# Optimization experiments

Hardware: AMD Instinct MI355X
Metric: run time of the kernel (lower is better)

Reference implementation:

```python
import jax, jax.numpy as jnp
import numpy as np

B, SQ, SKV, D, H = 2, 2048, 2048, 1024, 16
DH = D // H


def setup_inputs() -> dict:
    key = jax.random.key(0)
    ks = jax.random.split(key, 4)
    s = 0.02
    return {
        "query_input": jax.random.normal(ks[0], (B, SQ, D), jnp.float32),
        "kv_input": jax.random.normal(ks[1], (B, SKV, D), jnp.float32),
        "Wq": jax.random.normal(ks[2], (D, D), jnp.float32) * s,
        "bq": jnp.zeros((D,), jnp.float32),
        "Wkv": jax.random.normal(ks[3], (D, 2 * D), jnp.float32) * s,
        "bkv": jnp.zeros((2 * D,), jnp.float32),
        "Wo": jax.random.normal(jax.random.fold_in(key, 7), (D, D), jnp.float32) * s,
        "bo": jnp.zeros((D,), jnp.float32),
    }


def reference(query_input, kv_input, Wq, bq, Wkv, bkv, Wo, bo):
    scale = 1.0 / jnp.sqrt(jnp.float32(DH))
    # Projections
    q = query_input @ Wq + bq                      # [B, SQ, D]
    kv = kv_input @ Wkv + bkv                      # [B, SKV, 2D]
    k, v = jnp.split(kv, 2, axis=-1)               # [B, SKV, D] each
    # Split heads: [B, H, S, DH]
    q = q.reshape(B, SQ, H, DH).transpose(0, 2, 1, 3)
    k = k.reshape(B, SKV, H, DH).transpose(0, 2, 1, 3)
    v = v.reshape(B, SKV, H, DH).transpose(0, 2, 1, 3)
    # Scores S = QK^T / sqrt(d_k)
    scores = jnp.einsum("bhqd,bhkd->bhqk", q, k) * scale
    attn = jax.nn.softmax(scores, axis=-1)
    out = jnp.einsum("bhqk,bhkd->bhqd", attn, v)   # [B, H, SQ, DH]
    out = out.transpose(0, 2, 1, 3).reshape(B, SQ, D)
    return out @ Wo + bo
```

## Files before the change

### kernel.cpp

```cpp
#include <hip/hip_runtime.h>

typedef unsigned short u16;
typedef unsigned int u32;
typedef __bf16 bf16x8 __attribute__((ext_vector_type(8)));
typedef __bf16 bf16x2 __attribute__((ext_vector_type(2)));
typedef float f32x4 __attribute__((ext_vector_type(4)));

#define QSCALE 0.18033688011112f

__device__ __forceinline__ u16 f2bf(float f) {
  u32 u = __builtin_bit_cast(u32, f);
  u += 0x7fffu + ((u >> 16) & 1u);
  return (u16)(u >> 16);
}

__device__ __forceinline__ u32 pkbf(float a, float b) {
  bf16x2 t = {(__bf16)a, (__bf16)b};
  return __builtin_bit_cast(u32, t);
}

__device__ __forceinline__ bf16x8 as_bf16x8(uint4 v) {
  return __builtin_bit_cast(bf16x8, v);
}

__device__ __forceinline__ void async16(const void* g, void* l) {
  __builtin_amdgcn_global_load_lds(
      (__attribute__((address_space(1))) void*)(g),
      (__attribute__((address_space(3))) void*)(l), 16, 0, 0);
}

__global__ void prep_kernel(const float* __restrict__ xq, const float* __restrict__ xkv,
                            const float* __restrict__ Wq, const float* __restrict__ Wkv,
                            const float* __restrict__ Wo,
                            u16* __restrict__ Xq16, u16* __restrict__ Xkv16,
                            u16* __restrict__ WqT, u16* __restrict__ WkvT,
                            u16* __restrict__ WoT) {
  const int bid = blockIdx.x, tid = threadIdx.x;
  if (bid < 8192) {
    int i = bid * 256 + tid;
    const float* s; u16* d; int j;
    if (i < 1048576) { s = xq; d = Xq16; j = i; }
    else             { s = xkv; d = Xkv16; j = i - 1048576; }
    float4 v = ((const float4*)s)[j];
    ushort4 o;
    o.x = f2bf(v.x); o.y = f2bf(v.y); o.z = f2bf(v.z); o.w = f2bf(v.w);
    ((ushort4*)d)[j] = o;
    return;
  }
  const int b2 = bid - 8192;
  const int z = b2 >> 11, rem = b2 & 2047;
  const int by = rem >> 6, bx = rem & 63;
  const float* src; u16* dst; int Nd;
  if (z == 0)      { src = Wq;  dst = WqT;  Nd = 1024; }
  else if (z == 1) { src = Wkv; dst = WkvT; Nd = 2048; }
  else             { src = Wo;  dst = WoT;  Nd = 1024; }
  const int n0 = bx * 32, k0 = by * 32;
  if (n0 >= Nd) return;
  __shared__ float tile[32][33];
  const int tx = tid & 31, ty = tid >> 5;
#pragma unroll
  for (int j = 0; j < 4; ++j)
    tile[ty + 8 * j][tx] = src[(size_t)(k0 + ty + 8 * j) * Nd + n0 + tx];
  __syncthreads();
#pragma unroll
  for (int j = 0; j < 4; ++j)
    dst[(size_t)(n0 + ty + 8 * j) * 1024 + k0 + tx] = f2bf(tile[tx][ty + 8 * j]);
}

template <int MI>
static __device__ __forceinline__ void gemm_core(
    const u16* __restrict__ A, const u16* __restrict__ Bt, int m0,
    uint4* sA, uint4* sB, f32x4 (*acc)[4]) {
  const int tid = threadIdx.x;
  const int wv = tid >> 6, lane = tid & 63;
  const int quad = lane >> 4, l16 = lane & 15;
  const int wm = (wv >> 1) * (MI * 16), wn = (wv & 1) * 64;

  const int ib0 = wv * 128 + lane, ib1 = ib0 + 64;
  const int br0 = ib0 >> 2, bc0 = (ib0 & 3) ^ ((br0 >> 1) & 3);
  const int br1 = ib1 >> 2, bc1 = (ib1 & 3) ^ ((br1 >> 1) & 3);
  const u16* gB0 = Bt + (size_t)br0 * 1024 + bc0 * 8;
  const u16* gB1 = Bt + (size_t)br1 * 1024 + bc1 * 8;

  const int ia0 = wv * (MI * 32) + lane;
  const int ar0 = ia0 >> 2, ac0 = (ia0 & 3) ^ ((ar0 >> 1) & 3);
  const u16* gA0 = A + (size_t)(m0 + ar0) * 1024 + ac0 * 8;
  const int ia1 = ia0 + 64;
  const int ar1 = ia1 >> 2, ac1 = (ia1 & 3) ^ ((ar1 >> 1) & 3);
  const u16* gA1 = A + (size_t)(m0 + ar1) * 1024 + ac1 * 8;
  uint4* sAw = sA + wv * (MI * 32);
  uint4* sBw = sB + wv * 128;

  for (int k0 = 0; k0 < 1024; k0 += 32) {
    __syncthreads();
    async16(gA0 + k0, sAw);
    if (MI == 4) async16(gA1 + k0, sAw + 64);
    async16(gB0 + k0, sBw);
    async16(gB1 + k0, sBw + 64);
    __syncthreads();

    bf16x8 af[MI], bfr[4];
#pragma unroll
    for (int mi = 0; mi < MI; ++mi) {
      int r = wm + mi * 16 + l16;
      af[mi] = as_bf16x8(sA[r * 4 + (quad ^ ((r >> 1) & 3))]);
    }
#pragma unroll
    for (int ni = 0; ni < 4; ++ni) {
      int r = wn + ni * 16 + l16;
      bfr[ni] = as_bf16x8(sB[r * 4 + (quad ^ ((r >> 1) & 3))]);
    }
#pragma unroll
    for (int mi = 0; mi < MI; ++mi)
#pragma unroll
      for (int ni = 0; ni < 4; ++ni)
        acc[mi][ni] = __builtin_amdgcn_mfma_f32_16x16x32_bf16(
            af[mi], bfr[ni], acc[mi][ni], 0, 0, 0);
  }
}

__global__ __launch_bounds__(256, 3) void gemm_qkv(
    const u16* __restrict__ Xq, const u16* __restrict__ Xkv,
    const u16* __restrict__ WqT, const u16* __restrict__ WkvT,
    const float* __restrict__ bq, const float* __restrict__ bkv,
    u16* __restrict__ Qd, u16* __restrict__ Kd, u16* __restrict__ Vd) {
  __shared__ uint4 sA[512], sB[512];
  f32x4 acc[4][4] = {};
  const int n0 = blockIdx.x * 128, m0 = blockIdx.y * 128;
  const u16* A = (n0 < 1024) ? Xq : Xkv;
  const u16* Bt = (n0 < 1024) ? (WqT + (size_t)n0 * 1024)
                              : (WkvT + (size_t)(n0 - 1024) * 1024);
  const float* bias = (n0 < 1024) ? (bq + n0) : (bkv + (n0 - 1024));
  gemm_core<4>(A, Bt, m0, sA, sB, acc);

  const int tid = threadIdx.x, wv = tid >> 6, lane = tid & 63;
  const int quad = lane >> 4, l16 = lane & 15;
  const int wm = (wv >> 1) * 64, wn = (wv & 1) * 64;
  const int bb = m0 >> 11;
  const int gmb = m0 + wm + quad * 4;
  const int ssb = (m0 & 2047) + wm + quad * 4;
#pragma unroll
  for (int ni = 0; ni < 4; ++ni) {
    const int gn = n0 + wn + ni * 16 + l16;
    const float bvn = bias[wn + ni * 16 + l16];
    if (gn < 1024) {
      u16* base = Qd + gn;
#pragma unroll
      for (int mi = 0; mi < 4; ++mi)
#pragma unroll
        for (int r = 0; r < 4; ++r)
          base[(size_t)(gmb + mi * 16 + r) * 1024] = f2bf((acc[mi][ni][r] + bvn) * QSCALE);
    } else if (gn < 2048) {
      u16* base = Kd + (gn - 1024);
#pragma unroll
      for (int mi = 0; mi < 4; ++mi)
#pragma unroll
        for (int r = 0; r < 4; ++r)
          base[(size_t)(gmb + mi * 16 + r) * 1024] = f2bf(acc[mi][ni][r] + bvn);
    } else {
      const int col = gn - 2048, hh = col >> 6, dh = col & 63;
      u16* base = Vd + ((size_t)(bb * 16 + hh) * 64 + dh) * 2048 + ssb;
#pragma unroll
      for (int mi = 0; mi < 4; ++mi) {
        ushort4 o;
        o.x = f2bf(acc[mi][ni][0] + bvn);
        o.y = f2bf(acc[mi][ni][1] + bvn);
        o.z = f2bf(acc[mi][ni][2] + bvn);
        o.w = f2bf(acc[mi][ni][3] + bvn);
        *(ushort4*)(base + mi * 16) = o;
      }
    }
  }
}

__global__ __launch_bounds__(256, 2) void flash_attn(
    const u16* __restrict__ Q, const u16* __restrict__ K,
    const u16* __restrict__ V, u16* __restrict__ O) {
  __shared__ uint4 sK[2][512];
  __shared__ uint4 sV[2][512];
  __shared__ __align__(16) u16 sP[4][32][72];

  const int tid = threadIdx.x;
  const int wv = tid >> 6, lane = tid & 63;
  const int quad = lane >> 4, l16 = lane & 15;
  const int hb = blockIdx.x & 31;
  const int q0 = (blockIdx.x >> 5) * 128;
  const int h = hb & 15, bz = hb >> 4;

  const u16* Qb = Q + ((size_t)(bz * 2048 + q0)) * 1024 + h * 64;
  const u16* Kb = K + ((size_t)(bz * 2048)) * 1024 + h * 64;
  const u16* Vb = V + ((size_t)(bz * 16 + h)) * 64 * 2048;

  bf16x8 qf[2][2];
#pragma unroll
  for (int rb = 0; rb < 2; ++rb) {
    const uint4* qp = (const uint4*)(Qb + (size_t)(wv * 32 + rb * 16 + l16) * 1024);
    qf[rb][0] = as_bf16x8(qp[quad]);
    qf[rb][1] = as_bf16x8(qp[4 + quad]);
  }

  f32x4 oacc[2][4] = {};
  f32x4 lsum[2] = {};
  const uint4 ones4 = {0x3F803F80u, 0x3F803F80u, 0x3F803F80u, 0x3F803F80u};
  const bf16x8 ones = as_bf16x8(ones4);

  const int i0 = wv * 128 + lane, i1 = i0 + 64;
  const int kr0 = i0 >> 3, kr1 = i1 >> 3;
  const int kck0 = (i0 & 7) ^ ((i0 >> 5) & 7);
  const int kck1 = (i1 & 7) ^ ((i1 >> 5) & 7);
  const int vck0 = (i0 & 7) ^ (kr0 & 7);
  const int vck1 = (i1 & 7) ^ (kr1 & 7);
  const u16* gK0 = Kb + (size_t)kr0 * 1024 + kck0 * 8;
  const u16* gK1 = Kb + (size_t)kr1 * 1024 + kck1 * 8;
  const u16* gV0 = Vb + (size_t)kr0 * 2048 + vck0 * 8;
  const u16* gV1 = Vb + (size_t)kr1 * 2048 + vck1 * 8;
  const int wo = wv * 128;

  async16(gK0, &sK[0][wo]);
  async16(gK1, &sK[0][wo + 64]);
  async16(gV0, &sV[0][wo]);
  async16(gV1, &sV[0][wo + 64]);

  for (int t = 0; t < 32; ++t) {
    const int cur = t & 1;
    __syncthreads();
    if (t < 31) {
      const int nxt = cur ^ 1;
      const size_t ko = (size_t)(t + 1) * 64 * 1024;
      const int vo = (t + 1) * 64;
      async16(gK0 + ko, &sK[nxt][wo]);
      async16(gK1 + ko, &sK[nxt][wo + 64]);
      async16(gV0 + vo, &sV[nxt][wo]);
      async16(gV1 + vo, &sV[nxt][wo + 64]);
    }
    const uint4* K_ = sK[cur];
    const uint4* V_ = sV[cur];

    bf16x8 bK0[4], bK1[4], vf0[4], vf1[4];
#pragma unroll
    for (int ni = 0; ni < 4; ++ni) {
      int rr = l16 * 4 + ni;
      bK0[ni] = as_bf16x8(K_[rr * 8 + (quad ^ (l16 & 7))]);
      bK1[ni] = as_bf16x8(K_[rr * 8 + ((4 + quad) ^ (l16 & 7))]);
      int vv = ni * 16 + l16;
      vf0[ni] = as_bf16x8(V_[vv * 8 + (quad ^ (vv & 7))]);
      vf1[ni] = as_bf16x8(V_[vv * 8 + ((4 + quad) ^ (vv & 7))]);
    }

#pragma unroll
    for (int rb = 0; rb < 2; ++rb) {
      f32x4 s4[4];
#pragma unroll
      for (int ni = 0; ni < 4; ++ni) {
        f32x4 a = {0.f, 0.f, 0.f, 0.f};
        a = __builtin_amdgcn_mfma_f32_16x16x32_bf16(qf[rb][0], bK0[ni], a, 0, 0, 0);
        a = __builtin_amdgcn_mfma_f32_16x16x32_bf16(qf[rb][1], bK1[ni], a, 0, 0, 0);
        s4[ni] = a;
      }
#pragma unroll
      for (int r = 0; r < 4; ++r) {
        uint2 pk;
        pk.x = pkbf(exp2f(s4[0][r]), exp2f(s4[1][r]));
        pk.y = pkbf(exp2f(s4[2][r]), exp2f(s4[3][r]));
        *(uint2*)&sP[wv][rb * 16 + quad * 4 + r][l16 * 4] = pk;
      }
    }
#pragma unroll
    for (int rb = 0; rb < 2; ++rb) {
      bf16x8 pf0 = as_bf16x8(*(const uint4*)&sP[wv][rb * 16 + l16][quad * 8]);
      bf16x8 pf1 = as_bf16x8(*(const uint4*)&sP[wv][rb * 16 + l16][32 + quad * 8]);
      lsum[rb] = __builtin_amdgcn_mfma_f32_16x16x32_bf16(pf0, ones, lsum[rb], 0, 0, 0);
      lsum[rb] = __builtin_amdgcn_mfma_f32_16x16x32_bf16(pf1, ones, lsum[rb], 0, 0, 0);
#pragma unroll
      for (int ni = 0; ni < 4; ++ni) {
        oacc[rb][ni] = __builtin_amdgcn_mfma_f32_16x16x32_bf16(pf0, vf0[ni], oacc[rb][ni], 0, 0, 0);
        oacc[rb][ni] = __builtin_amdgcn_mfma_f32_16x16x32_bf16(pf1, vf1[ni], oacc[rb][ni], 0, 0, 0);
      }
    }
  }

#pragma unroll
  for (int rb = 0; rb < 2; ++rb) {
    u16* Ob = O + ((size_t)(bz * 2048 + q0 + wv * 32 + rb * 16 + quad * 4)) * 1024
                + h * 64;
#pragma unroll
    for (int r = 0; r < 4; ++r) {
      float rl = 1.0f / lsum[rb][r];
#pragma unroll
      for (int ni = 0; ni < 4; ++ni)
        Ob[(size_t)r * 1024 + ni * 16 + l16] = f2bf(oacc[rb][ni][r] * rl);
    }
  }
}

__global__ __launch_bounds__(256, 2) void gemm_out(
    const u16* __restrict__ A, const u16* __restrict__ Bt,
    const float* __restrict__ bias, float* __restrict__ C) {
  __shared__ uint4 sA[256], sB[512];
  f32x4 acc[2][4] = {};
  const int n0 = blockIdx.x * 128, m0 = blockIdx.y * 64;
  gemm_core<2>(A, Bt + (size_t)n0 * 1024, m0, sA, sB, acc);

  const int tid = threadIdx.x, wv = tid >> 6, lane = tid & 63;
  const int quad = lane >> 4, l16 = lane & 15;
  const int wm = (wv >> 1) * 32, wn = (wv & 1) * 64;
  float bv[4];
#pragma unroll
  for (int ni = 0; ni < 4; ++ni) bv[ni] = bias[n0 + wn + ni * 16 + l16];
#pragma unroll
  for (int mi = 0; mi < 2; ++mi)
#pragma unroll
    for (int ni = 0; ni < 4; ++ni)
#pragma unroll
      for (int r = 0; r < 4; ++r) {
        int gm = m0 + wm + mi * 16 + quad * 4 + r;
        int gn = n0 + wn + ni * 16 + l16;
        C[(size_t)gm * 1024 + gn] = acc[mi][ni][r] + bv[ni];
      }
}

extern "C" void kernel_launch(void* const* d_in, const int* in_sizes, int n_in,
                              void* d_out, int out_size, void* d_ws, size_t ws_size,
                              hipStream_t stream) {
  const float* xq  = (const float*)d_in[0];
  const float* xkv = (const float*)d_in[1];
  const float* Wq  = (const float*)d_in[2];
  const float* bq  = (const float*)d_in[3];
  const float* Wkv = (const float*)d_in[4];
  const float* bkv = (const float*)d_in[5];
  const float* Wo  = (const float*)d_in[6];
  const float* bo  = (const float*)d_in[7];
  float* out = (float*)d_out;

  char* p = (char*)d_ws;
  u16* Xq16  = (u16*)p; p += (size_t)8 << 20;
  u16* Xkv16 = (u16*)p; p += (size_t)8 << 20;
  u16* WqT   = (u16*)p; p += (size_t)2 << 20;
  u16* WkvT  = (u16*)p; p += (size_t)4 << 20;
  u16* WoT   = (u16*)p; p += (size_t)2 << 20;
  u16* Q16   = (u16*)p; p += (size_t)8 << 20;
  u16* K16   = (u16*)p; p += (size_t)8 << 20;
  u16* Vt16  = (u16*)p; p += (size_t)8 << 20;
  u16* O16   = (u16*)p; p += (size_t)8 << 20;

  prep_kernel<<<14336, 256, 0, stream>>>(xq, xkv, Wq, Wkv, Wo,
                                         Xq16, Xkv16, WqT, WkvT, WoT);
  gemm_qkv<<<dim3(24, 32), 256, 0, stream>>>(Xq16, Xkv16, WqT, WkvT, bq, bkv,
                                             Q16, K16, Vt16);
  flash_attn<<<512, 256, 0, stream>>>(Q16, K16, Vt16, O16);
  gemm_out<<<dim3(8, 64), 256, 0, stream>>>(O16, WoT, bo, out);
}
```

Measured before the change: 210.2 us.

## Software-pipeline PV matmul one tile behind QK and exp in flash attention

Restructures the attention loop so the P·V MFMAs for the previous KV tile run while the current tile's QK scores are exponentiated. P is double-buffered in shared memory and the V fragments are carried in registers across iterations. s_setprio is raised around the MFMA block, and the loop is unrolled by two. The aim is to overlap the transcendental and VALU work with matrix-core work, at the cost of more registers (extra V fragments) and more LDS, which may reduce occupancy.

```diff
diff --git a/kernel.cpp b/kernel.cpp
--- a/kernel.cpp
+++ b/kernel.cpp
@@ -178,7 +178,7 @@
     const u16* __restrict__ V, u16* __restrict__ O) {
   __shared__ uint4 sK[2][512];
   __shared__ uint4 sV[2][512];
-  __shared__ __align__(16) u16 sP[4][32][72];
+  __shared__ __align__(16) u16 sP[2][4][32][72];
 
   const int tid = threadIdx.x;
   const int wv = tid >> 6, lane = tid & 63;
@@ -221,6 +221,9 @@
   async16(gV0, &sV[0][wo]);
   async16(gV1, &sV[0][wo + 64]);
 
+  bf16x8 vfp0[4], vfp1[4];
+
+#pragma unroll 2
   for (int t = 0; t < 32; ++t) {
     const int cur = t & 1;
     __syncthreads();
@@ -236,48 +239,76 @@
     const uint4* K_ = sK[cur];
     const uint4* V_ = sV[cur];
 
-    bf16x8 bK0[4], bK1[4], vf0[4], vf1[4];
-#pragma unroll
-    for (int ni = 0; ni < 4; ++ni) {
-      int rr = l16 * 4 + ni;
-      bK0[ni] = as_bf16x8(K_[rr * 8 + (quad ^ (l16 & 7))]);
-      bK1[ni] = as_bf16x8(K_[rr * 8 + ((4 + quad) ^ (l16 & 7))]);
-      int vv = ni * 16 + l16;
-      vf0[ni] = as_bf16x8(V_[vv * 8 + (quad ^ (vv & 7))]);
-      vf1[ni] = as_bf16x8(V_[vv * 8 + ((4 + quad) ^ (vv & 7))]);
-    }
-
-#pragma unroll
-    for (int rb = 0; rb < 2; ++rb) {
-      f32x4 s4[4];
+    bf16x8 vn0[4], vn1[4];
+    f32x4 s4[2][4];
+    {
+      bf16x8 bK0[4], bK1[4];
 #pragma unroll
       for (int ni = 0; ni < 4; ++ni) {
-        f32x4 a = {0.f, 0.f, 0.f, 0.f};
-        a = __builtin_amdgcn_mfma_f32_16x16x32_bf16(qf[rb][0], bK0[ni], a, 0, 0, 0);
-        a = __builtin_amdgcn_mfma_f32_16x16x32_bf16(qf[rb][1], bK1[ni], a, 0, 0, 0);
-        s4[ni] = a;
-      }
+        int rr = l16 * 4 + ni;
+        bK0[ni] = as_bf16x8(K_[rr * 8 + (quad ^ (l16 & 7))]);
+        bK1[ni] = as_bf16x8(K_[rr * 8 + ((4 + quad) ^ (l16 & 7))]);
+        int vv = ni * 16 + l16;
+        vn0[ni] = as_bf16x8(V_[vv * 8 + (quad ^ (vv & 7))]);
+        vn1[ni] = as_bf16x8(V_[vv * 8 + ((4 + quad) ^ (vv & 7))]);
+      }
+
+#pragma unroll
+      for (int rb = 0; rb < 2; ++rb)
+#pragma unroll
+        for (int ni = 0; ni < 4; ++ni) {
+          f32x4 a = {0.f, 0.f, 0.f, 0.f};
+          a = __builtin_amdgcn_mfma_f32_16x16x32_bf16(qf[rb][0], bK0[ni], a, 0, 0, 0);
+          a = __builtin_amdgcn_mfma_f32_16x16x32_bf16(qf[rb][1], bK1[ni], a, 0, 0, 0);
+          s4[rb][ni] = a;
+        }
+    }
+
+    if (t) {
+      __builtin_amdgcn_s_setprio(1);
+#pragma unroll
+      for (int rb = 0; rb < 2; ++rb) {
+        bf16x8 pf0 = as_bf16x8(*(const uint4*)&sP[cur ^ 1][wv][rb * 16 + l16][quad * 8]);
+        bf16x8 pf1 = as_bf16x8(*(const uint4*)&sP[cur ^ 1][wv][rb * 16 + l16][32 + quad * 8]);
+        lsum[rb] = __builtin_amdgcn_mfma_f32_16x16x32_bf16(pf0, ones, lsum[rb], 0, 0, 0);
+        lsum[rb] = __builtin_amdgcn_mfma_f32_16x16x32_bf16(pf1, ones, lsum[rb], 0, 0, 0);
+#pragma unroll
+        for (int ni = 0; ni < 4; ++ni) {
+          oacc[rb][ni] = __builtin_amdgcn_mfma_f32_16x16x32_bf16(pf0, vfp0[ni], oacc[rb][ni], 0, 0, 0);
+          oacc[rb][ni] = __builtin_amdgcn_mfma_f32_16x16x32_bf16(pf1, vfp1[ni], oacc[rb][ni], 0, 0, 0);
+        }
+      }
+      __builtin_amdgcn_s_setprio(0);
+    }
+
+#pragma unroll
+    for (int rb = 0; rb < 2; ++rb)
 #pragma unroll
       for (int r = 0; r < 4; ++r) {
         uint2 pk;
-        pk.x = pkbf(exp2f(s4[0][r]), exp2f(s4[1][r]));
-        pk.y = pkbf(exp2f(s4[2][r]), exp2f(s4[3][r]));
-        *(uint2*)&sP[wv][rb * 16 + quad * 4 + r][l16 * 4] = pk;
-      }
-    }
-#pragma unroll
-    for (int rb = 0; rb < 2; ++rb) {
-      bf16x8 pf0 = as_bf16x8(*(const uint4*)&sP[wv][rb * 16 + l16][quad * 8]);
-      bf16x8 pf1 = as_bf16x8(*(const uint4*)&sP[wv][rb * 16 + l16][32 + quad * 8]);
-      lsum[rb] = __builtin_amdgcn_mfma_f32_16x16x32_bf16(pf0, ones, lsum[rb], 0, 0, 0);
-      lsum[rb] = __builtin_amdgcn_mfma_f32_16x16x32_bf16(pf1, ones, lsum[rb], 0, 0, 0);
-#pragma unroll
-      for (int ni = 0; ni < 4; ++ni) {
-        oacc[rb][ni] = __builtin_amdgcn_mfma_f32_16x16x32_bf16(pf0, vf0[ni], oacc[rb][ni], 0, 0, 0);
-        oacc[rb][ni] = __builtin_amdgcn_mfma_f32_16x16x32_bf16(pf1, vf1[ni], oacc[rb][ni], 0, 0, 0);
-      }
-    }
-  }
+        pk.x = pkbf(exp2f(s4[rb][0][r]), exp2f(s4[rb][1][r]));
+        pk.y = pkbf(exp2f(s4[rb][2][r]), exp2f(s4[rb][3][r]));
+        *(uint2*)&sP[cur][wv][rb * 16 + quad * 4 + r][l16 * 4] = pk;
+      }
+
+#pragma unroll
+    for (int ni = 0; ni < 4; ++ni) { vfp0[ni] = vn0[ni]; vfp1[ni] = vn1[ni]; }
+  }
+
+  __builtin_amdgcn_s_setprio(1);
+#pragma unroll
+  for (int rb = 0; rb < 2; ++rb) {
+    bf16x8 pf0 = as_bf16x8(*(const uint4*)&sP[1][wv][rb * 16 + l16][quad * 8]);
+    bf16x8 pf1 = as_bf16x8(*(const uint4*)&sP[1][wv][rb * 16 + l16][32 + quad * 8]);
+    lsum[rb] = __builtin_amdgcn_mfma_f32_16x16x32_bf16(pf0, ones, lsum[rb], 0, 0, 0);
+    lsum[rb] = __builtin_amdgcn_mfma_f32_16x16x32_bf16(pf1, ones, lsum[rb], 0, 0, 0);
+#pragma unroll
+    for (int ni = 0; ni < 4; ++ni) {
+      oacc[rb][ni] = __builtin_amdgcn_mfma_f32_16x16x32_bf16(pf0, vfp0[ni], oacc[rb][ni], 0, 0, 0);
+      oacc[rb][ni] = __builtin_amdgcn_mfma_f32_16x16x32_bf16(pf1, vfp1[ni], oacc[rb][ni], 0, 0, 0);
+    }
+  }
+  __builtin_amdgcn_s_setprio(0);
 
 #pragma unroll
   for (int rb = 0; rb < 2; ++rb) {
```

After: 207.1 us. About the same (-1.5%).

## Warp-specialize flash attention into QK/softmax producers and PV consumer waves

Applied to the files above, without the earlier changes.

Doubles the flash attention block to 512 threads. Four waves load K and compute QK^T plus exp into a double-buffered P tile, while four other waves load V and run the PV and row-sum MFMAs one tile behind at raised priority. The aim is to overlap the exp/softmax work with the PV matrix multiplies across waves. In exchange it adds shared memory for the second P buffer, needs an extra drain step after the loop, and with 512 blocks of 512 threads on the device it may lower the number of resident blocks.

```diff
diff --git a/kernel.cpp b/kernel.cpp
--- a/kernel.cpp
+++ b/kernel.cpp
@@ -173,15 +173,17 @@
   }
 }
 
-__global__ __launch_bounds__(256, 2) void flash_attn(
+__global__ __launch_bounds__(512, 4) void flash_attn(
     const u16* __restrict__ Q, const u16* __restrict__ K,
     const u16* __restrict__ V, u16* __restrict__ O) {
   __shared__ uint4 sK[2][512];
   __shared__ uint4 sV[2][512];
-  __shared__ __align__(16) u16 sP[4][32][72];
+  __shared__ __align__(16) u16 sP[2][4][32][72];
 
   const int tid = threadIdx.x;
   const int wv = tid >> 6, lane = tid & 63;
+  const int wg = wv & 3;
+  const bool prod = wv < 4;
   const int quad = lane >> 4, l16 = lane & 15;
   const int hb = blockIdx.x & 31;
   const int q0 = (blockIdx.x >> 5) * 128;
@@ -191,84 +193,121 @@
   const u16* Kb = K + ((size_t)(bz * 2048)) * 1024 + h * 64;
   const u16* Vb = V + ((size_t)(bz * 16 + h)) * 64 * 2048;
 
+  const int i0 = wg * 128 + lane, i1 = i0 + 64;
+  const int kr0 = i0 >> 3, kr1 = i1 >> 3;
+  const int wo = wg * 128;
+
   bf16x8 qf[2][2];
-#pragma unroll
-  for (int rb = 0; rb < 2; ++rb) {
-    const uint4* qp = (const uint4*)(Qb + (size_t)(wv * 32 + rb * 16 + l16) * 1024);
-    qf[rb][0] = as_bf16x8(qp[quad]);
-    qf[rb][1] = as_bf16x8(qp[4 + quad]);
-  }
-
+  const u16 *gK0 = nullptr, *gK1 = nullptr;
   f32x4 oacc[2][4] = {};
   f32x4 lsum[2] = {};
   const uint4 ones4 = {0x3F803F80u, 0x3F803F80u, 0x3F803F80u, 0x3F803F80u};
   const bf16x8 ones = as_bf16x8(ones4);
-
-  const int i0 = wv * 128 + lane, i1 = i0 + 64;
-  const int kr0 = i0 >> 3, kr1 = i1 >> 3;
-  const int kck0 = (i0 & 7) ^ ((i0 >> 5) & 7);
-  const int kck1 = (i1 & 7) ^ ((i1 >> 5) & 7);
-  const int vck0 = (i0 & 7) ^ (kr0 & 7);
-  const int vck1 = (i1 & 7) ^ (kr1 & 7);
-  const u16* gK0 = Kb + (size_t)kr0 * 1024 + kck0 * 8;
-  const u16* gK1 = Kb + (size_t)kr1 * 1024 + kck1 * 8;
-  const u16* gV0 = Vb + (size_t)kr0 * 2048 + vck0 * 8;
-  const u16* gV1 = Vb + (size_t)kr1 * 2048 + vck1 * 8;
-  const int wo = wv * 128;
-
-  async16(gK0, &sK[0][wo]);
-  async16(gK1, &sK[0][wo + 64]);
-  async16(gV0, &sV[0][wo]);
-  async16(gV1, &sV[0][wo + 64]);
-
+  const u16 *gV0 = nullptr, *gV1 = nullptr;
+
+  if (prod) {
+    const int kck0 = (i0 & 7) ^ ((i0 >> 5) & 7);
+    const int kck1 = (i1 & 7) ^ ((i1 >> 5) & 7);
+    gK0 = Kb + (size_t)kr0 * 1024 + kck0 * 8;
+    gK1 = Kb + (size_t)kr1 * 1024 + kck1 * 8;
+#pragma unroll
+    for (int rb = 0; rb < 2; ++rb) {
+      const uint4* qp = (const uint4*)(Qb + (size_t)(wg * 32 + rb * 16 + l16) * 1024);
+      qf[rb][0] = as_bf16x8(qp[quad]);
+      qf[rb][1] = as_bf16x8(qp[4 + quad]);
+    }
+    async16(gK0, &sK[0][wo]);
+    async16(gK1, &sK[0][wo + 64]);
+  } else {
+    const int vck0 = (i0 & 7) ^ (kr0 & 7);
+    const int vck1 = (i1 & 7) ^ (kr1 & 7);
+    gV0 = Vb + (size_t)kr0 * 2048 + vck0 * 8;
+    gV1 = Vb + (size_t)kr1 * 2048 + vck1 * 8;
+  }
+
+#pragma unroll 2
   for (int t = 0; t < 32; ++t) {
     const int cur = t & 1;
     __syncthreads();
-    if (t < 31) {
-      const int nxt = cur ^ 1;
-      const size_t ko = (size_t)(t + 1) * 64 * 1024;
-      const int vo = (t + 1) * 64;
-      async16(gK0 + ko, &sK[nxt][wo]);
-      async16(gK1 + ko, &sK[nxt][wo + 64]);
-      async16(gV0 + vo, &sV[nxt][wo]);
-      async16(gV1 + vo, &sV[nxt][wo + 64]);
-    }
-    const uint4* K_ = sK[cur];
-    const uint4* V_ = sV[cur];
-
-    bf16x8 bK0[4], bK1[4], vf0[4], vf1[4];
+
+    if (prod) {
+      if (t < 31) {
+        const size_t ko = (size_t)(t + 1) * 64 * 1024;
+        async16(gK0 + ko, &sK[cur ^ 1][wo]);
+        async16(gK1 + ko, &sK[cur ^ 1][wo + 64]);
+      }
+      const uint4* K_ = sK[cur];
+      bf16x8 bK0[4], bK1[4];
+#pragma unroll
+      for (int ni = 0; ni < 4; ++ni) {
+        int rr = l16 * 4 + ni;
+        bK0[ni] = as_bf16x8(K_[rr * 8 + (quad ^ (l16 & 7))]);
+        bK1[ni] = as_bf16x8(K_[rr * 8 + ((4 + quad) ^ (l16 & 7))]);
+      }
+#pragma unroll
+      for (int rb = 0; rb < 2; ++rb) {
+        f32x4 s4[4];
+#pragma unroll
+        for (int ni = 0; ni < 4; ++ni) {
+          f32x4 a = {0.f, 0.f, 0.f, 0.f};
+          a = __builtin_amdgcn_mfma_f32_16x16x32_bf16(qf[rb][0], bK0[ni], a, 0, 0, 0);
+          a = __builtin_amdgcn_mfma_f32_16x16x32_bf16(qf[rb][1], bK1[ni], a, 0, 0, 0);
+          s4[ni] = a;
+        }
+#pragma unroll
+        for (int r = 0; r < 4; ++r) {
+          uint2 pk;
+          pk.x = pkbf(exp2f(s4[0][r]), exp2f(s4[1][r]));
+          pk.y = pkbf(exp2f(s4[2][r]), exp2f(s4[3][r]));
+          *(uint2*)&sP[cur][wg][rb * 16 + quad * 4 + r][l16 * 4] = pk;
+        }
+      }
+    } else {
+      const int vo = t * 64;
+      async16(gV0 + vo, &sV[cur][wo]);
+      async16(gV1 + vo, &sV[cur][wo + 64]);
+      if (t) {
+        const uint4* V_ = sV[cur ^ 1];
+        bf16x8 vf0[4], vf1[4];
+#pragma unroll
+        for (int ni = 0; ni < 4; ++ni) {
+          int vvv = ni * 16 + l16;
+          vf0[ni] = as_bf16x8(V_[vvv * 8 + (quad ^ (vvv & 7))]);
+          vf1[ni] = as_bf16x8(V_[vvv * 8 + ((4 + quad) ^ (vvv & 7))]);
+        }
+        __builtin_amdgcn_s_setprio(1);
+#pragma unroll
+        for (int rb = 0; rb < 2; ++rb) {
+          bf16x8 pf0 = as_bf16x8(*(const uint4*)&sP[cur ^ 1][wg][rb * 16 + l16][quad * 8]);
+          bf16x8 pf1 = as_bf16x8(*(const uint4*)&sP[cur ^ 1][wg][rb * 16 + l16][32 + quad * 8]);
+          lsum[rb] = __builtin_amdgcn_mfma_f32_16x16x32_bf16(pf0, ones, lsum[rb], 0, 0, 0);
+          lsum[rb] = __builtin_amdgcn_mfma_f32_16x16x32_bf16(pf1, ones, lsum[rb], 0, 0, 0);
+#pragma unroll
+          for (int ni = 0; ni < 4; ++ni) {
+            oacc[rb][ni] = __builtin_amdgcn_mfma_f32_16x16x32_bf16(pf0, vf0[ni], oacc[rb][ni], 0, 0, 0);
+            oacc[rb][ni] = __builtin_amdgcn_mfma_f32_16x16x32_bf16(pf1, vf1[ni], oacc[rb][ni], 0, 0, 0);
+          }
+        }
+        __builtin_amdgcn_s_setprio(0);
+      }
+    }
+  }
+
+  __syncthreads();
+  if (!prod) {
+    const uint4* V_ = sV[1];
+    bf16x8 vf0[4], vf1[4];
 #pragma unroll
     for (int ni = 0; ni < 4; ++ni) {
-      int rr = l16 * 4 + ni;
-      bK0[ni] = as_bf16x8(K_[rr * 8 + (quad ^ (l16 & 7))]);
-      bK1[ni] = as_bf16x8(K_[rr * 8 + ((4 + quad) ^ (l16 & 7))]);
-      int vv = ni * 16 + l16;
-      vf0[ni] = as_bf16x8(V_[vv * 8 + (quad ^ (vv & 7))]);
-      vf1[ni] = as_bf16x8(V_[vv * 8 + ((4 + quad) ^ (vv & 7))]);
-    }
-
+      int vvv = ni * 16 + l16;
+      vf0[ni] = as_bf16x8(V_[vvv * 8 + (quad ^ (vvv & 7))]);
+      vf1[ni] = as_bf16x8(V_[vvv * 8 + ((4 + quad) ^ (vvv & 7))]);
+    }
+    __builtin_amdgcn_s_setprio(1);
 #pragma unroll
     for (int rb = 0; rb < 2; ++rb) {
-      f32x4 s4[4];
-#pragma unroll
-      for (int ni = 0; ni < 4; ++ni) {
-        f32x4 a = {0.f, 0.f, 0.f, 0.f};
-        a = __builtin_amdgcn_mfma_f32_16x16x32_bf16(qf[rb][0], bK0[ni], a, 0, 0, 0);
-        a = __builtin_amdgcn_mfma_f32_16x16x32_bf16(qf[rb][1], bK1[ni], a, 0, 0, 0);
-        s4[ni] = a;
-      }
-#pragma unroll
-      for (int r = 0; r < 4; ++r) {
-        uint2 pk;
-        pk.x = pkbf(exp2f(s4[0][r]), exp2f(s4[1][r]));
-        pk.y = pkbf(exp2f(s4[2][r]), exp2f(s4[3][r]));
-        *(uint2*)&sP[wv][rb * 16 + quad * 4 + r][l16 * 4] = pk;
-      }
-    }
-#pragma unroll
-    for (int rb = 0; rb < 2; ++rb) {
-      bf16x8 pf0 = as_bf16x8(*(const uint4*)&sP[wv][rb * 16 + l16][quad * 8]);
-      bf16x8 pf1 = as_bf16x8(*(const uint4*)&sP[wv][rb * 16 + l16][32 + quad * 8]);
+      bf16x8 pf0 = as_bf16x8(*(const uint4*)&sP[1][wg][rb * 16 + l16][quad * 8]);
+      bf16x8 pf1 = as_bf16x8(*(const uint4*)&sP[1][wg][rb * 16 + l16][32 + quad * 8]);
       lsum[rb] = __builtin_amdgcn_mfma_f32_16x16x32_bf16(pf0, ones, lsum[rb], 0, 0, 0);
       lsum[rb] = __builtin_amdgcn_mfma_f32_16x16x32_bf16(pf1, ones, lsum[rb], 0, 0, 0);
 #pragma unroll
@@ -277,18 +316,19 @@
         oacc[rb][ni] = __builtin_amdgcn_mfma_f32_16x16x32_bf16(pf1, vf1[ni], oacc[rb][ni], 0, 0, 0);
       }
     }
-  }
-
-#pragma unroll
-  for (int rb = 0; rb < 2; ++rb) {
-    u16* Ob = O + ((size_t)(bz * 2048 + q0 + wv * 32 + rb * 16 + quad * 4)) * 1024
-                + h * 64;
-#pragma unroll
-    for (int r = 0; r < 4; ++r) {
-      float rl = 1.0f / lsum[rb][r];
-#pragma unroll
-      for (int ni = 0; ni < 4; ++ni)
-        Ob[(size_t)r * 1024 + ni * 16 + l16] = f2bf(oacc[rb][ni][r] * rl);
+    __builtin_amdgcn_s_setprio(0);
+
+#pragma unroll
+    for (int rb = 0; rb < 2; ++rb) {
+      u16* Ob = O + ((size_t)(bz * 2048 + q0 + wg * 32 + rb * 16 + quad * 4)) * 1024
+                  + h * 64;
+#pragma unroll
+      for (int r = 0; r < 4; ++r) {
+        float rl = 1.0f / lsum[rb][r];
+#pragma unroll
+        for (int ni = 0; ni < 4; ++ni)
+          Ob[(size_t)r * 1024 + ni * 16 + l16] = f2bf(oacc[rb][ni][r] * rl);
+      }
     }
   }
 }
@@ -347,6 +387,6 @@
                                          Xq16, Xkv16, WqT, WkvT, WoT);
   gemm_qkv<<<dim3(24, 32), 256, 0, stream>>>(Xq16, Xkv16, WqT, WkvT, bq, bkv,
                                              Q16, K16, Vt16);
-  flash_attn<<<512, 256, 0, stream>>>(Q16, K16, Vt16, O16);
+  flash_attn<<<512, 512, 0, stream>>>(Q16, K16, Vt16, O16);
   gemm_out<<<dim3(8, 64), 256, 0, stream>>>(O16, WoT, bo, out);
 }
```

After: 211.8 us. No clear change (+0.7%).

## Rewrite flash attention with 32x32x16 MFMA, transposed scores, register-resident P

Applied to the files above, without the earlier changes.

The attention kernel now computes S^T = K·Q^T with 32x32x16 bf16 MFMAs, so the exponentiated scores can be repacked into the A-operand layout for the PV product using v_permlane32_swap instead of a round trip through shared memory. Row sums are accumulated in registers rather than by an extra MFMA against a ones vector. Each block now handles 256 query rows, with 64 per wave, and the launch is halved to 256 blocks with occupancy hint 1. The intent is to cut LDS traffic and instruction count and to raise MFMA efficiency. The cost is fewer blocks (256) on a large GPU and higher register pressure.

```diff
diff --git a/kernel.cpp b/kernel.cpp
--- a/kernel.cpp
+++ b/kernel.cpp
@@ -5,6 +5,7 @@
 typedef __bf16 bf16x8 __attribute__((ext_vector_type(8)));
 typedef __bf16 bf16x2 __attribute__((ext_vector_type(2)));
 typedef float f32x4 __attribute__((ext_vector_type(4)));
+typedef float f32x16 __attribute__((ext_vector_type(16)));
 
 #define QSCALE 0.18033688011112f
 
@@ -173,48 +174,44 @@
   }
 }
 
-__global__ __launch_bounds__(256, 2) void flash_attn(
+__global__ __launch_bounds__(256, 1) void flash_attn(
     const u16* __restrict__ Q, const u16* __restrict__ K,
     const u16* __restrict__ V, u16* __restrict__ O) {
   __shared__ uint4 sK[2][512];
   __shared__ uint4 sV[2][512];
-  __shared__ __align__(16) u16 sP[4][32][72];
+  __shared__ float sL[256];
 
   const int tid = threadIdx.x;
   const int wv = tid >> 6, lane = tid & 63;
-  const int quad = lane >> 4, l16 = lane & 15;
+  const int c = lane & 31, hh = lane >> 5;
   const int hb = blockIdx.x & 31;
-  const int q0 = (blockIdx.x >> 5) * 128;
+  const int q0 = (blockIdx.x >> 5) * 256;
   const int h = hb & 15, bz = hb >> 4;
 
-  const u16* Qb = Q + ((size_t)(bz * 2048 + q0)) * 1024 + h * 64;
+  const u16* Qb = Q + ((size_t)(bz * 2048 + q0 + wv * 64)) * 1024 + h * 64;
   const u16* Kb = K + ((size_t)(bz * 2048)) * 1024 + h * 64;
   const u16* Vb = V + ((size_t)(bz * 16 + h)) * 64 * 2048;
 
-  bf16x8 qf[2][2];
-#pragma unroll
-  for (int rb = 0; rb < 2; ++rb) {
-    const uint4* qp = (const uint4*)(Qb + (size_t)(wv * 32 + rb * 16 + l16) * 1024);
-    qf[rb][0] = as_bf16x8(qp[quad]);
-    qf[rb][1] = as_bf16x8(qp[4 + quad]);
-  }
-
-  f32x4 oacc[2][4] = {};
-  f32x4 lsum[2] = {};
-  const uint4 ones4 = {0x3F803F80u, 0x3F803F80u, 0x3F803F80u, 0x3F803F80u};
-  const bf16x8 ones = as_bf16x8(ones4);
-
   const int i0 = wv * 128 + lane, i1 = i0 + 64;
-  const int kr0 = i0 >> 3, kr1 = i1 >> 3;
-  const int kck0 = (i0 & 7) ^ ((i0 >> 5) & 7);
-  const int kck1 = (i1 & 7) ^ ((i1 >> 5) & 7);
-  const int vck0 = (i0 & 7) ^ (kr0 & 7);
-  const int vck1 = (i1 & 7) ^ (kr1 & 7);
-  const u16* gK0 = Kb + (size_t)kr0 * 1024 + kck0 * 8;
-  const u16* gK1 = Kb + (size_t)kr1 * 1024 + kck1 * 8;
-  const u16* gV0 = Vb + (size_t)kr0 * 2048 + vck0 * 8;
-  const u16* gV1 = Vb + (size_t)kr1 * 2048 + vck1 * 8;
+  const int r0 = i0 >> 3, r1 = i1 >> 3;
+  const int ck0 = (i0 & 7) ^ (r0 & 7), ck1 = (i1 & 7) ^ (r1 & 7);
+  const u16* gK0 = Kb + (size_t)r0 * 1024 + ck0 * 8;
+  const u16* gK1 = Kb + (size_t)r1 * 1024 + ck1 * 8;
+  const u16* gV0 = Vb + (size_t)r0 * 2048 + ck0 * 8;
+  const u16* gV1 = Vb + (size_t)r1 * 2048 + ck1 * 8;
   const int wo = wv * 128;
+
+  bf16x8 qf[2][4];
+#pragma unroll
+  for (int g = 0; g < 2; ++g) {
+    const u16* qr = Qb + (size_t)(32 * g + c) * 1024 + hh * 8;
+#pragma unroll
+    for (int s = 0; s < 4; ++s)
+      qf[g][s] = as_bf16x8(*(const uint4*)(qr + 16 * s));
+  }
+
+  f32x16 oacc[2][2] = {};
+  float lp[2] = {0.f, 0.f};
 
   async16(gK0, &sK[0][wo]);
   async16(gK1, &sK[0][wo + 64]);
@@ -225,71 +222,88 @@
     const int cur = t & 1;
     __syncthreads();
     if (t < 31) {
-      const int nxt = cur ^ 1;
       const size_t ko = (size_t)(t + 1) * 64 * 1024;
       const int vo = (t + 1) * 64;
-      async16(gK0 + ko, &sK[nxt][wo]);
-      async16(gK1 + ko, &sK[nxt][wo + 64]);
-      async16(gV0 + vo, &sV[nxt][wo]);
-      async16(gV1 + vo, &sV[nxt][wo + 64]);
+      async16(gK0 + ko, &sK[cur ^ 1][wo]);
+      async16(gK1 + ko, &sK[cur ^ 1][wo + 64]);
+      async16(gV0 + vo, &sV[cur ^ 1][wo]);
+      async16(gV1 + vo, &sV[cur ^ 1][wo + 64]);
     }
     const uint4* K_ = sK[cur];
     const uint4* V_ = sV[cur];
 
-    bf16x8 bK0[4], bK1[4], vf0[4], vf1[4];
-#pragma unroll
-    for (int ni = 0; ni < 4; ++ni) {
-      int rr = l16 * 4 + ni;
-      bK0[ni] = as_bf16x8(K_[rr * 8 + (quad ^ (l16 & 7))]);
-      bK1[ni] = as_bf16x8(K_[rr * 8 + ((4 + quad) ^ (l16 & 7))]);
-      int vv = ni * 16 + l16;
-      vf0[ni] = as_bf16x8(V_[vv * 8 + (quad ^ (vv & 7))]);
-      vf1[ni] = as_bf16x8(V_[vv * 8 + ((4 + quad) ^ (vv & 7))]);
-    }
-
-#pragma unroll
-    for (int rb = 0; rb < 2; ++rb) {
-      f32x4 s4[4];
-#pragma unroll
-      for (int ni = 0; ni < 4; ++ni) {
-        f32x4 a = {0.f, 0.f, 0.f, 0.f};
-        a = __builtin_amdgcn_mfma_f32_16x16x32_bf16(qf[rb][0], bK0[ni], a, 0, 0, 0);
-        a = __builtin_amdgcn_mfma_f32_16x16x32_bf16(qf[rb][1], bK1[ni], a, 0, 0, 0);
-        s4[ni] = a;
-      }
-#pragma unroll
-      for (int r = 0; r < 4; ++r) {
-        uint2 pk;
-        pk.x = pkbf(exp2f(s4[0][r]), exp2f(s4[1][r]));
-        pk.y = pkbf(exp2f(s4[2][r]), exp2f(s4[3][r]));
-        *(uint2*)&sP[wv][rb * 16 + quad * 4 + r][l16 * 4] = pk;
-      }
-    }
-#pragma unroll
-    for (int rb = 0; rb < 2; ++rb) {
-      bf16x8 pf0 = as_bf16x8(*(const uint4*)&sP[wv][rb * 16 + l16][quad * 8]);
-      bf16x8 pf1 = as_bf16x8(*(const uint4*)&sP[wv][rb * 16 + l16][32 + quad * 8]);
-      lsum[rb] = __builtin_amdgcn_mfma_f32_16x16x32_bf16(pf0, ones, lsum[rb], 0, 0, 0);
-      lsum[rb] = __builtin_amdgcn_mfma_f32_16x16x32_bf16(pf1, ones, lsum[rb], 0, 0, 0);
-#pragma unroll
-      for (int ni = 0; ni < 4; ++ni) {
-        oacc[rb][ni] = __builtin_amdgcn_mfma_f32_16x16x32_bf16(pf0, vf0[ni], oacc[rb][ni], 0, 0, 0);
-        oacc[rb][ni] = __builtin_amdgcn_mfma_f32_16x16x32_bf16(pf1, vf1[ni], oacc[rb][ni], 0, 0, 0);
-      }
-    }
-  }
-
-#pragma unroll
-  for (int rb = 0; rb < 2; ++rb) {
-    u16* Ob = O + ((size_t)(bz * 2048 + q0 + wv * 32 + rb * 16 + quad * 4)) * 1024
-                + h * 64;
-#pragma unroll
-    for (int r = 0; r < 4; ++r) {
-      float rl = 1.0f / lsum[rb][r];
-#pragma unroll
-      for (int ni = 0; ni < 4; ++ni)
-        Ob[(size_t)r * 1024 + ni * 16 + l16] = f2bf(oacc[rb][ni][r] * rl);
-    }
+    bf16x8 kf[2][4], vf[2][4];
+#pragma unroll
+    for (int b = 0; b < 2; ++b) {
+      const int row = 32 * b + c, sw = row & 7;
+#pragma unroll
+      for (int s = 0; s < 4; ++s) {
+        kf[b][s] = as_bf16x8(K_[row * 8 + ((2 * s + hh) ^ sw)]);
+        vf[b][s] = as_bf16x8(V_[row * 8 + ((2 * s + hh) ^ sw)]);
+      }
+    }
+
+    bf16x8 pa[2][4];
+#pragma unroll
+    for (int b = 0; b < 2; ++b)
+#pragma unroll
+      for (int g = 0; g < 2; ++g) {
+        f32x16 sAcc = {};
+#pragma unroll
+        for (int s = 0; s < 4; ++s)
+          sAcc = __builtin_amdgcn_mfma_f32_32x32x16_bf16(kf[b][s], qf[g][s], sAcc, 0, 0, 0);
+        float e[16];
+#pragma unroll
+        for (int r = 0; r < 16; ++r) e[r] = __builtin_amdgcn_exp2f(sAcc[r]);
+        float t0 = (e[0] + e[1]) + (e[2] + e[3]);
+        float t1 = (e[4] + e[5]) + (e[6] + e[7]);
+        float t2 = (e[8] + e[9]) + (e[10] + e[11]);
+        float t3 = (e[12] + e[13]) + (e[14] + e[15]);
+        lp[g] += (t0 + t1) + (t2 + t3);
+        u32 wA0 = pkbf(e[0], e[1]),   wA1 = pkbf(e[2], e[3]);
+        u32 wB0 = pkbf(e[4], e[5]),   wB1 = pkbf(e[6], e[7]);
+        u32 wC0 = pkbf(e[8], e[9]),   wC1 = pkbf(e[10], e[11]);
+        u32 wD0 = pkbf(e[12], e[13]), wD1 = pkbf(e[14], e[15]);
+        asm("v_permlane32_swap_b32 %0, %1" : "+v"(wA0), "+v"(wB0));
+        asm("v_permlane32_swap_b32 %0, %1" : "+v"(wA1), "+v"(wB1));
+        asm("v_permlane32_swap_b32 %0, %1" : "+v"(wC0), "+v"(wD0));
+        asm("v_permlane32_swap_b32 %0, %1" : "+v"(wC1), "+v"(wD1));
+        uint4 f0 = {wA0, wA1, wB0, wB1};
+        uint4 f1 = {wC0, wC1, wD0, wD1};
+        pa[g][2 * b]     = as_bf16x8(f0);
+        pa[g][2 * b + 1] = as_bf16x8(f1);
+      }
+
+#pragma unroll
+    for (int g = 0; g < 2; ++g)
+#pragma unroll
+      for (int nb = 0; nb < 2; ++nb)
+#pragma unroll
+        for (int ks = 0; ks < 4; ++ks)
+          oacc[g][nb] = __builtin_amdgcn_mfma_f32_32x32x16_bf16(
+              pa[g][ks], vf[nb][ks], oacc[g][nb], 0, 0, 0);
+  }
+
+#pragma unroll
+  for (int g = 0; g < 2; ++g) {
+    u32 a = __builtin_bit_cast(u32, lp[g]);
+    u32 b = a;
+    asm("v_permlane32_swap_b32 %0, %1" : "+v"(a), "+v"(b));
+    float tot = __builtin_bit_cast(float, a) + __builtin_bit_cast(float, b);
+    sL[wv * 64 + 32 * g + c] = 1.0f / tot;
+  }
+
+#pragma unroll
+  for (int g = 0; g < 2; ++g) {
+    u16* Ob = O + ((size_t)(bz * 2048 + q0 + wv * 64 + 32 * g)) * 1024 + h * 64;
+#pragma unroll
+    for (int nb = 0; nb < 2; ++nb)
+#pragma unroll
+      for (int r = 0; r < 16; ++r) {
+        const int qr = (r & 3) + 8 * (r >> 2) + 4 * hh;
+        float rl = sL[wv * 64 + 32 * g + qr];
+        Ob[(size_t)qr * 1024 + nb * 32 + c] = f2bf(oacc[g][nb][r] * rl);
+      }
   }
 }
 
@@ -347,6 +361,6 @@
                                          Xq16, Xkv16, WqT, WkvT, WoT);
   gemm_qkv<<<dim3(24, 32), 256, 0, stream>>>(Xq16, Xkv16, WqT, WkvT, bq, bkv,
                                              Q16, K16, Vt16);
-  flash_attn<<<512, 256, 0, stream>>>(Q16, K16, Vt16, O16);
+  flash_attn<<<256, 256, 0, stream>>>(Q16, K16, Vt16, O16);
   gemm_out<<<dim3(8, 64), 256, 0, stream>>>(O16, WoT, bo, out);
 }
```

Measured after the change: 210.7 us. About the same (+0.2%).
